# Optimization experiments

Hardware: AMD Instinct MI355X
Metric: run time of the kernel (lower is better)

## Reference

```python
import jax, jax.numpy as jnp
import numpy as np

B = 4_194_304  # batch
M = 4          # num_modes
N = 4          # num_nodes (hardcoded in BistableModeBank)
MU_MIN, MU_MAX = 0.1, 1.5


def setup_inputs() -> dict:
    key = jax.random.key(0)
    k1, k2, k3, k4, k5, k6 = jax.random.split(key, 6)
    return {
        "X": jax.random.normal(k1, (B, N), dtype=jnp.float32),
        "z": jax.random.randint(k2, (B,), 0, M, dtype=jnp.int32),
        "dt_val": jnp.full((1,), 0.01, dtype=jnp.float32),
        # learned params (torch inits them to zeros; small noise for non-degenerate test)
        "graph_logits": 0.1 * jax.random.normal(k3, (M, N, N), dtype=jnp.float32),
        "mu_logits": 0.1 * jax.random.normal(k4, (M, N), dtype=jnp.float32),
        "alpha_param": 0.1 * jax.random.normal(k5, (M,), dtype=jnp.float32),
        "beta_param": 0.1 * jax.random.normal(k6, (M,), dtype=jnp.float32),
    }


def reference(X, z, dt_val, graph_logits, mu_logits, alpha_param, beta_param):
    # graphs(): symmetrize logits, sigmoid, zero diagonal
    S = 0.5 * (graph_logits + jnp.swapaxes(graph_logits, 1, 2))
    W = jax.nn.sigmoid(S) * (1.0 - jnp.eye(N, dtype=X.dtype))  # (M,N,N)
    mus = MU_MIN + (MU_MAX - MU_MIN) * jax.nn.sigmoid(mu_logits)  # (M,N)
    deg = W.sum(axis=-1)  # (M,N)

    # per-item mode routing (replaces boolean-mask gather/scatter of forward_grouped)
    mu_z = mus[z]                        # (B,N)
    deg_z = deg[z]                       # (B,N)
    a_z = alpha_param[z][:, None]        # (B,1)
    b_z = beta_param[z][:, None]         # (B,1)

    local = mu_z * X - X ** 3            # bistable_batch
    # adjacency matmul for all modes, then select routed mode per item
    coup_all = jnp.einsum('mij,bj->bmi', W, X)                       # (B,M,N)
    coup_z = jnp.take_along_axis(coup_all, z[:, None, None], axis=1)[:, 0, :]  # (B,N)

    coupling = a_z * deg_z * X + b_z * coup_z
    dt = dt_val[0]
    return X + dt * (local + coupling)
```

## Files before the change

kernel.cpp:

```cpp
#include <hip/hip_runtime.h>


__global__ __launch_bounds__(256) void bistable_kernel(
    const float* __restrict__ X,
    const int*   __restrict__ z,
    const float* __restrict__ dt_val,
    const float* __restrict__ G,
    const float* __restrict__ mu_logits,
    const float* __restrict__ alpha_p,
    const float* __restrict__ beta_p,
    float* __restrict__ out,
    int Bn)
{
    __shared__ float A[4 * 16];
    __shared__ float s_dt;

    const int t = threadIdx.x;
    if (t < 16) {
        const int m = t >> 2;
        const int i = t & 3;
        const float dt = dt_val[0];
        float w[4];
        float deg = 0.0f;
        #pragma unroll
        for (int j = 0; j < 4; ++j) {
            float s = 0.5f * (G[m * 16 + i * 4 + j] + G[m * 16 + j * 4 + i]);
            float wv = 1.0f / (1.0f + __expf(-s));
            if (j == i) wv = 0.0f;
            w[j] = wv;
            deg += wv;
        }
        const float mu = 0.1f + 1.4f / (1.0f + __expf(-mu_logits[m * 4 + i]));
        const float a = alpha_p[m];
        const float b = beta_p[m];
        float arow[4];
        #pragma unroll
        for (int j = 0; j < 4; ++j) arow[j] = dt * b * w[j];
        arow[i] = 1.0f + dt * (mu + a * deg);
        #pragma unroll
        for (int j = 0; j < 4; ++j) A[m * 16 + i * 4 + j] = arow[j];
    }
    if (t == 0) s_dt = dt_val[0];
    __syncthreads();

    const float dt = s_dt;
    const float4* __restrict__ X4 = (const float4*)X;
    float4* __restrict__ O4 = (float4*)out;

    const int tid = blockIdx.x * blockDim.x + t;
    const int stride = gridDim.x * blockDim.x;
    for (int idx = tid; idx < Bn; idx += stride) {
        const float4 xv = X4[idx];
        const int m = z[idx];
        const float* __restrict__ a = &A[m * 16];
        const float x0 = xv.x, x1 = xv.y, x2 = xv.z, x3 = xv.w;

        float o0 = a[0]  * x0 + a[1]  * x1 + a[2]  * x2 + a[3]  * x3;
        float o1 = a[4]  * x0 + a[5]  * x1 + a[6]  * x2 + a[7]  * x3;
        float o2 = a[8]  * x0 + a[9]  * x1 + a[10] * x2 + a[11] * x3;
        float o3 = a[12] * x0 + a[13] * x1 + a[14] * x2 + a[15] * x3;

        o0 -= dt * x0 * x0 * x0;
        o1 -= dt * x1 * x1 * x1;
        o2 -= dt * x2 * x2 * x2;
        o3 -= dt * x3 * x3 * x3;

        O4[idx] = make_float4(o0, o1, o2, o3);
    }
}

extern "C" void kernel_launch(void* const* d_in, const int* in_sizes, int n_in,
                              void* d_out, int out_size, void* d_ws, size_t ws_size,
                              hipStream_t stream) {
    const float* X         = (const float*)d_in[0];
    const int*   z         = (const int*)d_in[1];
    const float* dt_val    = (const float*)d_in[2];
    const float* G         = (const float*)d_in[3];
    const float* mu_logits = (const float*)d_in[4];
    const float* alpha_p   = (const float*)d_in[5];
    const float* beta_p    = (const float*)d_in[6];
    float* out = (float*)d_out;

    const int Bn = in_sizes[1];

    const int block = 256;
    int grid = (Bn + block - 1) / block;
    if (grid > 2048) grid = 2048;

    bistable_kernel<<<grid, block, 0, stream>>>(X, z, dt_val, G, mu_logits,
                                                alpha_p, beta_p, out, Bn);
}
```

Before: 29.10 us.

## Use one element per thread, issue loads before table setup, nontemporal stores

Replaces the grid-stride loop over 2048 blocks with one thread per batch item across the full grid. Each thread issues its X and z loads before the shared mode-table setup and the barrier, so global memory latency overlaps with the table computation. Output is written with nontemporal stores to limit cache pollution. In exchange, every one of the 16K blocks recomputes the small table (transcendentals plus a barrier), which adds redundant work per block.

```diff
diff --git a/kernel.cpp b/kernel.cpp
--- a/kernel.cpp
+++ b/kernel.cpp
@@ -1,5 +1,7 @@
 #include <hip/hip_runtime.h>
 
+
+typedef float fvec4 __attribute__((ext_vector_type(4)));
 
 __global__ __launch_bounds__(256) void bistable_kernel(
     const float* __restrict__ X,
@@ -13,60 +15,55 @@
     int Bn)
 {
     __shared__ float A[4 * 16];
-    __shared__ float s_dt;
 
     const int t = threadIdx.x;
+    const int idx = blockIdx.x * 256 + t;
+
+    fvec4 xv;
+    int m = 0;
+    const bool valid = (idx < Bn);
+    if (valid) {
+        xv = ((const fvec4*)X)[idx];
+        m = z[idx];
+    }
+    const float dt = dt_val[0];
+
     if (t < 16) {
-        const int m = t >> 2;
-        const int i = t & 3;
-        const float dt = dt_val[0];
+        const int mm = t >> 2;
+        const int i  = t & 3;
         float w[4];
         float deg = 0.0f;
         #pragma unroll
         for (int j = 0; j < 4; ++j) {
-            float s = 0.5f * (G[m * 16 + i * 4 + j] + G[m * 16 + j * 4 + i]);
+            float s = 0.5f * (G[mm * 16 + i * 4 + j] + G[mm * 16 + j * 4 + i]);
             float wv = 1.0f / (1.0f + __expf(-s));
             if (j == i) wv = 0.0f;
             w[j] = wv;
             deg += wv;
         }
-        const float mu = 0.1f + 1.4f / (1.0f + __expf(-mu_logits[m * 4 + i]));
-        const float a = alpha_p[m];
-        const float b = beta_p[m];
+        const float mu = 0.1f + 1.4f / (1.0f + __expf(-mu_logits[mm * 4 + i]));
+        const float a = alpha_p[mm];
+        const float b = beta_p[mm];
         float arow[4];
         #pragma unroll
         for (int j = 0; j < 4; ++j) arow[j] = dt * b * w[j];
         arow[i] = 1.0f + dt * (mu + a * deg);
         #pragma unroll
-        for (int j = 0; j < 4; ++j) A[m * 16 + i * 4 + j] = arow[j];
+        for (int j = 0; j < 4; ++j) A[mm * 16 + i * 4 + j] = arow[j];
     }
-    if (t == 0) s_dt = dt_val[0];
     __syncthreads();
 
-    const float dt = s_dt;
-    const float4* __restrict__ X4 = (const float4*)X;
-    float4* __restrict__ O4 = (float4*)out;
+    if (!valid) return;
 
-    const int tid = blockIdx.x * blockDim.x + t;
-    const int stride = gridDim.x * blockDim.x;
-    for (int idx = tid; idx < Bn; idx += stride) {
-        const float4 xv = X4[idx];
-        const int m = z[idx];
-        const float* __restrict__ a = &A[m * 16];
-        const float x0 = xv.x, x1 = xv.y, x2 = xv.z, x3 = xv.w;
+    const float* __restrict__ a = &A[m * 16];
+    const float x0 = xv.x, x1 = xv.y, x2 = xv.z, x3 = xv.w;
+    fvec4 ov;
+    ov.x = a[0]  * x0 + a[1]  * x1 + a[2]  * x2 + a[3]  * x3 - dt * x0 * x0 * x0;
+    ov.y = a[4]  * x0 + a[5]  * x1 + a[6]  * x2 + a[7]  * x3 - dt * x1 * x1 * x1;
+    ov.z = a[8]  * x0 + a[9]  * x1 + a[10] * x2 + a[11] * x3 - dt * x2 * x2 * x2;
+    ov.w = a[12] * x0 + a[13] * x1 + a[14] * x2 + a[15] * x3 - dt * x3 * x3 * x3;
 
-        float o0 = a[0]  * x0 + a[1]  * x1 + a[2]  * x2 + a[3]  * x3;
-        float o1 = a[4]  * x0 + a[5]  * x1 + a[6]  * x2 + a[7]  * x3;
-        float o2 = a[8]  * x0 + a[9]  * x1 + a[10] * x2 + a[11] * x3;
-        float o3 = a[12] * x0 + a[13] * x1 + a[14] * x2 + a[15] * x3;
-
-        o0 -= dt * x0 * x0 * x0;
-        o1 -= dt * x1 * x1 * x1;
-        o2 -= dt * x2 * x2 * x2;
-        o3 -= dt * x3 * x3 * x3;
-
-        O4[idx] = make_float4(o0, o1, o2, o3);
-    }
+    __builtin_nontemporal_store(ov, &((fvec4*)out)[idx]);
 }
 
 extern "C" void kernel_launch(void* const* d_in, const int* in_sizes, int n_in,
@@ -84,8 +81,7 @@
     const int Bn = in_sizes[1];
 
     const int block = 256;
-    int grid = (Bn + block - 1) / block;
-    if (grid > 2048) grid = 2048;
+    const int grid = (Bn + block - 1) / block;
 
     bistable_kernel<<<grid, block, 0, stream>>>(X, z, dt_val, G, mu_logits,
                                                 alpha_p, beta_p, out, Bn);
```

After: 29.21 us. Within noise of the previous version (+0.3%).
